# Kernel optimization log

Measured on AMD Instinct MI355X. Metric: run time of the kernel, lower is better.

Reference implementation:

```python
import jax, jax.numpy as jnp
import numpy as np

N_NODES = 100000
N_EDGES = 1600000
D_IN = 128
D_HID = 64


def setup_inputs() -> dict:
    key = jax.random.key(0)
    k1, k2, k3, k4 = jax.random.split(key, 4)
    x = jax.random.normal(k1, (N_NODES, D_IN), dtype=jnp.float32)
    edge_index = jax.random.randint(k2, (2, N_EDGES), 0, N_NODES, dtype=jnp.int64)
    W1 = jax.random.normal(k3, (D_IN, D_HID), dtype=jnp.float32) / np.sqrt(D_IN)
    b1 = jnp.zeros((D_HID,), dtype=jnp.float32)
    W2 = jax.random.normal(k4, (D_HID, 1), dtype=jnp.float32) / np.sqrt(D_HID)
    b2 = jnp.zeros((1,), dtype=jnp.float32)
    return {"x": x, "edge_index": edge_index, "W1": W1, "b1": b1, "W2": W2, "b2": b2}


def _gcn_layer(x, W, b, src, dst, norm, n):
    # PyG GCNConv: linear transform, then normalized scatter-add aggregation, then bias
    h = x @ W                                   # [N, d_out]
    msg = h[src] * norm[:, None]                # gather + edge-weight   [E', d_out]
    out = jax.ops.segment_sum(msg, dst, num_segments=n)  # scatter-add
    return out + b


def reference(x, edge_index, W1, b1, W2, b2):
    n = x.shape[0]
    loops = jnp.arange(n, dtype=edge_index.dtype)
    src = jnp.concatenate([edge_index[0], loops])  # self-loops added (GCN default)
    dst = jnp.concatenate([edge_index[1], loops])
    # symmetric normalization: deg^{-1/2}[src] * deg^{-1/2}[dst]
    deg = jax.ops.segment_sum(jnp.ones(dst.shape, x.dtype), dst, num_segments=n)
    dis = jnp.where(deg > 0, jax.lax.rsqrt(jnp.maximum(deg, 1e-12)), 0.0)
    norm = dis[src] * dis[dst]
    h = jax.nn.relu(_gcn_layer(x, W1, b1, src, dst, norm, n))
    y = _gcn_layer(h, W2, b2, src, dst, norm, n)   # [N, 1]
    # ConstantPad1d((0, num_node_features-1), 0) -> [N, D_IN]
    return jnp.pad(y, ((0, 0), (0, x.shape[1] - 1)))
```

## Files before the change

### kernel.cpp

```cpp
#include <hip/hip_runtime.h>

#define N_NODES 100000
#define N_EDGES 1600000
#define D_IN 128
#define D_HID 64

#define BKT_SHIFT 8
#define BKT_NODES 256
#define NB 391
#define NBLK 392
#define SLOT 32
#define SEG4 (SLOT / 4)
#define REG4 (NBLK * SEG4)
#define BKT_CAP 5120
#define OVF_CAP 8192

#define EST 512
#define BST 1024

typedef __attribute__((ext_vector_type(8))) short bf16x8;
typedef __attribute__((ext_vector_type(4))) float f32x4;

__device__ __forceinline__ unsigned short f2b(float f) {
    union { float f; unsigned u; } c; c.f = f;
    unsigned r = (c.u + 0x7FFFu + ((c.u >> 16) & 1u)) >> 16;
    return (unsigned short)r;
}
__device__ __forceinline__ float blo(unsigned u) { return __uint_as_float(u << 16); }
__device__ __forceinline__ float bhi(unsigned u) { return __uint_as_float(u & 0xffff0000u); }

__global__ __launch_bounds__(256) void k_prep(const float* __restrict__ W1,
                                              unsigned short* __restrict__ w1t,
                                              int* __restrict__ ovf_cnt) {
    int t = blockIdx.x * 256 + threadIdx.x;
    if (t == 0) ovf_cnt[0] = 0;
    int k = t >> 6, f = t & 63;
    w1t[f * D_IN + k] = f2b(W1[t]);
}

__global__ __launch_bounds__(EST) void k_escatter(const int* __restrict__ src,
                                                  const int* __restrict__ dst,
                                                  int* __restrict__ pairs,
                                                  int* __restrict__ cnt_blk,
                                                  int* __restrict__ ovf_cnt,
                                                  int2* __restrict__ ovf, int E) {
    __shared__ int lcur[NB];
    __shared__ int lp[NB * SLOT];
    int tid = threadIdx.x;
    for (int t = tid; t < NB; t += EST) lcur[t] = 0;
    __syncthreads();
    int chunk = (E + NBLK - 1) / NBLK;
    int beg = blockIdx.x * chunk;
    int end = min(beg + chunk, E);
    for (int e = beg + tid; e < end; e += EST) {
        int d = dst[e], s = src[e];
        int bk = d >> BKT_SHIFT;
        int slot = atomicAdd(&lcur[bk], 1);
        if (slot < SLOT)
            lp[(bk << 5) + slot] = (s << BKT_SHIFT) | (d & (BKT_NODES - 1));
        else {
            int o = atomicAdd(ovf_cnt, 1);
            if (o < OVF_CAP) ovf[o] = make_int2(s, d);
        }
    }
    __syncthreads();
    uint4* p4 = (uint4*)pairs;
    const uint4* lp4 = (const uint4*)lp;
    for (int i4 = tid; i4 < NB * SEG4; i4 += EST) {
        int bk = i4 >> 3;
        int c = min(lcur[bk], SLOT);
        if (((i4 & 7) << 2) < c)
            p4[((size_t)bk * NBLK + blockIdx.x) * SEG4 + (i4 & 7)] = lp4[i4];
    }
    for (int t = tid; t < NB; t += EST)
        cnt_blk[t * NBLK + blockIdx.x] = min(lcur[t], SLOT);
}

__global__ __launch_bounds__(BST) void k_bsort(const uint4* __restrict__ pairs4,
                                               const int* __restrict__ cnt_blk,
                                               const int* __restrict__ ovf_cnt,
                                               const int2* __restrict__ ovf,
                                               int* __restrict__ srcs_sorted,
                                               int* __restrict__ row_start,
                                               int* __restrict__ row_end,
                                               float* __restrict__ dis, int n) {
    __shared__ uint4 reg4[REG4];
    __shared__ int segc[NBLK];
    __shared__ int cnt[BKT_NODES];
    __shared__ int exc[BKT_NODES];
    __shared__ int sorted[BKT_CAP];
    __shared__ int nE_sh;
    int b = blockIdx.x;
    int tid = threadIdx.x;
    int node0 = b << BKT_SHIFT;
    int ocnt = min(ovf_cnt[0], OVF_CAP);
    const uint4* region = pairs4 + (size_t)b * REG4;

    for (int i = tid; i < NBLK; i += BST) segc[i] = cnt_blk[b * NBLK + i];
    if (tid < BKT_NODES) cnt[tid] = 0;
    __syncthreads();

    for (int i4 = tid; i4 < REG4; i4 += BST) {
        int c = segc[i4 >> 3];
        int k = (i4 & 7) * 4;
        if (k < c) {
            uint4 v = region[i4];
            reg4[i4] = v;
            atomicAdd(&cnt[v.x & (BKT_NODES - 1)], 1);
            if (k + 1 < c) atomicAdd(&cnt[v.y & (BKT_NODES - 1)], 1);
            if (k + 2 < c) atomicAdd(&cnt[v.z & (BKT_NODES - 1)], 1);
            if (k + 3 < c) atomicAdd(&cnt[v.w & (BKT_NODES - 1)], 1);
        }
    }
    for (int k = tid; k < ocnt; k += BST) {
        int2 e = ovf[k];
        if ((e.y >> BKT_SHIFT) == b) atomicAdd(&cnt[e.y & (BKT_NODES - 1)], 1);
    }
    __syncthreads();

    if (tid < 64) {
        int run = 0;
        for (int c = 0; c < BKT_NODES; c += 64) {
            int v = cnt[c + tid];
            int inc = v;
            for (int off = 1; off < 64; off <<= 1) {
                int t2 = __shfl_up(inc, off);
                if (tid >= off) inc += t2;
            }
            exc[c + tid] = run + inc - v;
            run += __shfl(inc, 63);
        }
        if (tid == 63) nE_sh = run;
    }
    __syncthreads();

    if (tid < BKT_NODES) {
        int node = node0 + tid;
        if (node < n) {
            int rs = b * BKT_CAP + exc[tid];
            row_start[node] = rs;
            row_end[node] = rs + cnt[tid];
            dis[node] = rsqrtf((float)cnt[tid] + 1.0f);
        }
    }
    int nE = nE_sh;
    __syncthreads();
    if (tid < BKT_NODES) cnt[tid] = exc[tid];
    __syncthreads();

    for (int i4 = tid; i4 < REG4; i4 += BST) {
        int c = segc[i4 >> 3];
        int k = (i4 & 7) * 4;
        if (k < c) {
            uint4 v = reg4[i4];
            { int p = atomicAdd(&cnt[v.x & (BKT_NODES - 1)], 1); sorted[p] = (int)(v.x >> 8); }
            if (k + 1 < c) { int p = atomicAdd(&cnt[v.y & (BKT_NODES - 1)], 1); sorted[p] = (int)(v.y >> 8); }
            if (k + 2 < c) { int p = atomicAdd(&cnt[v.z & (BKT_NODES - 1)], 1); sorted[p] = (int)(v.z >> 8); }
            if (k + 3 < c) { int p = atomicAdd(&cnt[v.w & (BKT_NODES - 1)], 1); sorted[p] = (int)(v.w >> 8); }
        }
    }
    for (int k = tid; k < ocnt; k += BST) {
        int2 e = ovf[k];
        if ((e.y >> BKT_SHIFT) == b) {
            int p = atomicAdd(&cnt[e.y & (BKT_NODES - 1)], 1);
            sorted[p] = e.x;
        }
    }
    __syncthreads();

    int gbase = b * BKT_CAP;
    for (int k = tid; k < nE; k += BST)
        srcs_sorted[gbase + k] = sorted[k];
}

#define LS 136
__global__ __launch_bounds__(256) void k_gemm1(const float* __restrict__ x,
                                               const uint4* __restrict__ w1t4,
                                               const float* __restrict__ dis,
                                               unsigned short* __restrict__ h1s, int n) {
    __shared__ unsigned short xs[64 * LS];
    __shared__ unsigned short ws[64 * LS];
    int tid = threadIdx.x;
    int node0 = blockIdx.x * 64;

#pragma unroll
    for (int it = 0; it < 4; ++it) {
        int e = tid + it * 256;
        int f = e >> 4, c = e & 15;
        *(uint4*)&ws[f * LS + c * 8] = w1t4[e];
    }
#pragma unroll
    for (int it = 0; it < 8; ++it) {
        int e4 = tid + it * 256;
        int node = e4 >> 5;
        int k = (e4 & 31) * 4;
        float4 v = make_float4(0.f, 0.f, 0.f, 0.f);
        if (node0 + node < n)
            v = ((const float4*)x)[((size_t)(node0 + node) * D_IN + k) >> 2];
        uint2 u;
        u.x = (unsigned)f2b(v.x) | ((unsigned)f2b(v.y) << 16);
        u.y = (unsigned)f2b(v.z) | ((unsigned)f2b(v.w) << 16);
        *(uint2*)&xs[node * LS + k] = u;
    }
    __syncthreads();

    int wv = tid >> 6;
    int lane = tid & 63;
    int m16 = lane & 15;
    int q = lane >> 4;

    bf16x8 afrag[4];
#pragma unroll
    for (int ks = 0; ks < 4; ++ks)
        afrag[ks] = *(const bf16x8*)&xs[(wv * 16 + m16) * LS + ks * 32 + q * 8];

    f32x4 acc[4];
#pragma unroll
    for (int ft = 0; ft < 4; ++ft) acc[ft] = (f32x4){0.f, 0.f, 0.f, 0.f};

#pragma unroll
    for (int ft = 0; ft < 4; ++ft)
#pragma unroll
        for (int ks = 0; ks < 4; ++ks) {
            bf16x8 bfrag = *(const bf16x8*)&ws[(ft * 16 + m16) * LS + ks * 32 + q * 8];
            acc[ft] = __builtin_amdgcn_mfma_f32_16x16x32_bf16(afrag[ks], bfrag, acc[ft], 0, 0, 0);
        }

#pragma unroll
    for (int r = 0; r < 4; ++r) {
        int node = node0 + wv * 16 + q * 4 + r;
        if (node < n) {
            float d = dis[node];
#pragma unroll
            for (int ft = 0; ft < 4; ++ft)
                h1s[(size_t)node * D_HID + ft * 16 + m16] = f2b(acc[ft][r] * d);
        }
    }
}

__global__ __launch_bounds__(256) void k_gather1(const int* __restrict__ srcs,
                                                 const int* __restrict__ row_start,
                                                 const int* __restrict__ row_end,
                                                 const float* __restrict__ dis,
                                                 const uint4* __restrict__ h4,
                                                 const float* __restrict__ b1,
                                                 const float* __restrict__ W2,
                                                 float* __restrict__ zd, int n) {
    int i = blockIdx.x * 8 + (threadIdx.x >> 5);
    int lane = threadIdx.x & 63;
    int g = (lane >> 3) & 3;
    int m8 = lane & 7;
    float dd = dis[i];

    float a0, a1, a2, a3, a4, a5, a6, a7;
    {
        uint4 u = h4[(unsigned)i * 8u + m8];
        float w = (g == 0) ? 1.f : 0.f;
        a0 = w * blo(u.x); a1 = w * bhi(u.x);
        a2 = w * blo(u.y); a3 = w * bhi(u.y);
        a4 = w * blo(u.z); a5 = w * bhi(u.z);
        a6 = w * blo(u.w); a7 = w * bhi(u.w);
    }

#define ACC(u) { a0 += blo(u.x); a1 += bhi(u.x); a2 += blo(u.y); a3 += bhi(u.y); \
                 a4 += blo(u.z); a5 += bhi(u.z); a6 += blo(u.w); a7 += bhi(u.w); }
    int end = row_end[i];
    int j = row_start[i] + g;
    for (; j + 12 < end; j += 16) {
        int s0 = srcs[j];
        int s1 = srcs[j + 4];
        int s2 = srcs[j + 8];
        int s3 = srcs[j + 12];
        uint4 u0 = h4[(unsigned)s0 * 8u + m8];
        uint4 u1 = h4[(unsigned)s1 * 8u + m8];
        uint4 u2 = h4[(unsigned)s2 * 8u + m8];
        uint4 u3 = h4[(unsigned)s3 * 8u + m8];
        ACC(u0); ACC(u1); ACC(u2); ACC(u3);
    }
    for (; j + 4 < end; j += 8) {
        int s0 = srcs[j];
        int s1 = srcs[j + 4];
        uint4 u0 = h4[(unsigned)s0 * 8u + m8];
        uint4 u1 = h4[(unsigned)s1 * 8u + m8];
        ACC(u0); ACC(u1);
    }
    if (j < end) {
        int s0 = srcs[j];
        uint4 u0 = h4[(unsigned)s0 * 8u + m8];
        ACC(u0);
    }
#undef ACC

#pragma unroll
    for (int off = 8; off < 32; off <<= 1) {
        a0 += __shfl_xor(a0, off); a1 += __shfl_xor(a1, off);
        a2 += __shfl_xor(a2, off); a3 += __shfl_xor(a3, off);
        a4 += __shfl_xor(a4, off); a5 += __shfl_xor(a5, off);
        a6 += __shfl_xor(a6, off); a7 += __shfl_xor(a7, off);
    }
    float4 ba = ((const float4*)b1)[m8 * 2];
    float4 bb = ((const float4*)b1)[m8 * 2 + 1];
    float4 wa = ((const float4*)W2)[m8 * 2];
    float4 wb = ((const float4*)W2)[m8 * 2 + 1];
    float v = fmaxf(fmaf(dd, a0, ba.x), 0.f) * wa.x + fmaxf(fmaf(dd, a1, ba.y), 0.f) * wa.y
            + fmaxf(fmaf(dd, a2, ba.z), 0.f) * wa.z + fmaxf(fmaf(dd, a3, ba.w), 0.f) * wa.w
            + fmaxf(fmaf(dd, a4, bb.x), 0.f) * wb.x + fmaxf(fmaf(dd, a5, bb.y), 0.f) * wb.y
            + fmaxf(fmaf(dd, a6, bb.z), 0.f) * wb.z + fmaxf(fmaf(dd, a7, bb.w), 0.f) * wb.w;
#pragma unroll
    for (int off = 1; off < 8; off <<= 1) v += __shfl_xor(v, off);
    if ((lane & 31) == 0) zd[i] = v * dd;
}

__global__ __launch_bounds__(256) void k_gather2(const int* __restrict__ srcs,
                                                 const int* __restrict__ row_start,
                                                 const int* __restrict__ row_end,
                                                 const float* __restrict__ dis,
                                                 const float* __restrict__ zd,
                                                 const float* __restrict__ b2,
                                                 float* __restrict__ out, int n) {
    int i = blockIdx.x * 8 + (threadIdx.x >> 5);
    int l = threadIdx.x & 31;
    float acc = 0.f;
    int beg = row_start[i], end = row_end[i];
    for (int j = beg + l; j < end; j += 32)
        acc += zd[srcs[j]];
#pragma unroll
    for (int off = 1; off < 32; off <<= 1) acc += __shfl_xor(acc, off);
    float y = (acc + zd[i]) * dis[i] + b2[0];
    float4 v = make_float4(0.f, 0.f, 0.f, 0.f);
    if (l == 0) v.x = y;
    ((float4*)out)[(size_t)i * 32 + l] = v;
}

extern "C" void kernel_launch(void* const* d_in, const int* in_sizes, int n_in,
                              void* d_out, int out_size, void* d_ws, size_t ws_size,
                              hipStream_t stream) {
    const float* x  = (const float*)d_in[0];
    const int*   ei = (const int*)d_in[1];
    const float* W1 = (const float*)d_in[2];
    const float* b1 = (const float*)d_in[3];
    const float* W2 = (const float*)d_in[4];
    const float* b2 = (const float*)d_in[5];
    float* out = (float*)d_out;

    const int n = N_NODES;
    const int E = N_EDGES;
    const int* src = ei;
    const int* dst = ei + E;

    int* pairs       = (int*)d_ws;
    int* cnt_blk     = pairs + (size_t)NB * NBLK * SLOT;
    int* srcs_sorted = cnt_blk + (size_t)NB * NBLK;
    int* row_start   = srcs_sorted + (size_t)NB * BKT_CAP;
    int* row_end     = row_start + n;
    int* ovf_cnt     = row_end + n;
    int2* ovf        = (int2*)(ovf_cnt + 4);
    float* dis       = (float*)(ovf + OVF_CAP);
    unsigned short* h1s = (unsigned short*)(dis + n);
    unsigned short* w1t = h1s + (size_t)n * D_HID;
    float* zd        = (float*)(w1t + D_IN * D_HID);

    k_prep<<<32, 256, 0, stream>>>(W1, w1t, ovf_cnt);
    k_escatter<<<NBLK, EST, 0, stream>>>(src, dst, pairs, cnt_blk, ovf_cnt, ovf, E);
    k_bsort<<<NB, BST, 0, stream>>>((const uint4*)pairs, cnt_blk, ovf_cnt, ovf,
                                    srcs_sorted, row_start, row_end, dis, n);

    k_gemm1<<<(n + 63) / 64, 256, 0, stream>>>(x, (const uint4*)w1t, dis, h1s, n);

    k_gather1<<<(n + 7) / 8, 256, 0, stream>>>(srcs_sorted, row_start, row_end, dis,
                                               (const uint4*)h1s, b1, W2, zd, n);
    k_gather2<<<(n + 7) / 8, 256, 0, stream>>>(srcs_sorted, row_start, row_end, dis,
                                               zd, b2, out, n);
}
```

Measured before the change: 195.3 us.

## Fuse edge scatter and GEMM into one launch, apply source norm in gather

The edge-bucketing scatter and the X·W1 bf16 MFMA GEMM now run as two block roles inside one kernel, so the GEMM no longer waits for the degree computation. To make that possible, the per-source dis scaling moves out of the GEMM epilogue and into gather1, which loads dis[src] per edge and uses FMA accumulation. The W1 transpose/convert prep kernel is folded into each GEMM block, and the overflow-counter reset becomes a memset. This removes two launches and overlaps independent work, at the cost of an extra scattered 4-byte load per edge in the gather and redundant W1 conversion in every GEMM block.

```diff
diff --git a/kernel.cpp b/kernel.cpp
--- a/kernel.cpp
+++ b/kernel.cpp
@@ -15,8 +15,9 @@
 #define BKT_CAP 5120
 #define OVF_CAP 8192
 
-#define EST 512
+#define FST 512
 #define BST 1024
+#define GEMM_NB 782
 
 typedef __attribute__((ext_vector_type(8))) short bf16x8;
 typedef __attribute__((ext_vector_type(4))) float f32x4;
@@ -29,51 +30,110 @@
 __device__ __forceinline__ float blo(unsigned u) { return __uint_as_float(u << 16); }
 __device__ __forceinline__ float bhi(unsigned u) { return __uint_as_float(u & 0xffff0000u); }
 
-__global__ __launch_bounds__(256) void k_prep(const float* __restrict__ W1,
-                                              unsigned short* __restrict__ w1t,
-                                              int* __restrict__ ovf_cnt) {
-    int t = blockIdx.x * 256 + threadIdx.x;
-    if (t == 0) ovf_cnt[0] = 0;
-    int k = t >> 6, f = t & 63;
-    w1t[f * D_IN + k] = f2b(W1[t]);
-}
-
-__global__ __launch_bounds__(EST) void k_escatter(const int* __restrict__ src,
-                                                  const int* __restrict__ dst,
-                                                  int* __restrict__ pairs,
-                                                  int* __restrict__ cnt_blk,
-                                                  int* __restrict__ ovf_cnt,
-                                                  int2* __restrict__ ovf, int E) {
-    __shared__ int lcur[NB];
-    __shared__ int lp[NB * SLOT];
+#define LS 136
+__global__ __launch_bounds__(FST) void k_fused(const int* __restrict__ src,
+                                               const int* __restrict__ dst,
+                                               int* __restrict__ pairs,
+                                               int* __restrict__ cnt_blk,
+                                               int* __restrict__ ovf_cnt,
+                                               int2* __restrict__ ovf, int E,
+                                               const float* __restrict__ x,
+                                               const float* __restrict__ W1,
+                                               unsigned short* __restrict__ h1s, int n) {
+    __shared__ __align__(16) unsigned char smem[52224];
     int tid = threadIdx.x;
-    for (int t = tid; t < NB; t += EST) lcur[t] = 0;
-    __syncthreads();
-    int chunk = (E + NBLK - 1) / NBLK;
-    int beg = blockIdx.x * chunk;
-    int end = min(beg + chunk, E);
-    for (int e = beg + tid; e < end; e += EST) {
-        int d = dst[e], s = src[e];
-        int bk = d >> BKT_SHIFT;
-        int slot = atomicAdd(&lcur[bk], 1);
-        if (slot < SLOT)
-            lp[(bk << 5) + slot] = (s << BKT_SHIFT) | (d & (BKT_NODES - 1));
-        else {
-            int o = atomicAdd(ovf_cnt, 1);
-            if (o < OVF_CAP) ovf[o] = make_int2(s, d);
-        }
-    }
-    __syncthreads();
-    uint4* p4 = (uint4*)pairs;
-    const uint4* lp4 = (const uint4*)lp;
-    for (int i4 = tid; i4 < NB * SEG4; i4 += EST) {
-        int bk = i4 >> 3;
-        int c = min(lcur[bk], SLOT);
-        if (((i4 & 7) << 2) < c)
-            p4[((size_t)bk * NBLK + blockIdx.x) * SEG4 + (i4 & 7)] = lp4[i4];
-    }
-    for (int t = tid; t < NB; t += EST)
-        cnt_blk[t * NBLK + blockIdx.x] = min(lcur[t], SLOT);
+
+    if (blockIdx.x < NBLK) {
+        int* lp   = (int*)smem;
+        int* lcur = lp + NB * SLOT;
+        for (int t = tid; t < NB; t += FST) lcur[t] = 0;
+        __syncthreads();
+        int chunk = (E + NBLK - 1) / NBLK;
+        int beg = blockIdx.x * chunk;
+        int end = min(beg + chunk, E);
+        for (int e = beg + tid; e < end; e += FST) {
+            int d = dst[e], s = src[e];
+            int bk = d >> BKT_SHIFT;
+            int slot = atomicAdd(&lcur[bk], 1);
+            if (slot < SLOT)
+                lp[(bk << 5) + slot] = (s << BKT_SHIFT) | (d & (BKT_NODES - 1));
+            else {
+                int o = atomicAdd(ovf_cnt, 1);
+                if (o < OVF_CAP) ovf[o] = make_int2(s, d);
+            }
+        }
+        __syncthreads();
+        uint4* p4 = (uint4*)pairs;
+        const uint4* lp4 = (const uint4*)lp;
+        for (int i4 = tid; i4 < NB * SEG4; i4 += FST) {
+            int bk = i4 >> 3;
+            int c = min(lcur[bk], SLOT);
+            if (((i4 & 7) << 2) < c)
+                p4[((size_t)bk * NBLK + blockIdx.x) * SEG4 + (i4 & 7)] = lp4[i4];
+        }
+        for (int t = tid; t < NB; t += FST)
+            cnt_blk[t * NBLK + blockIdx.x] = min(lcur[t], SLOT);
+    } else {
+        unsigned short* ws = (unsigned short*)smem;
+        unsigned short* xs = ws + 64 * LS;
+        int half = tid >> 8;
+        int t2 = tid & 255;
+        int node0 = (blockIdx.x - NBLK) * 128 + half * 64;
+        unsigned short* xsh = xs + half * 64 * LS;
+
+#pragma unroll
+        for (int it = 0; it < 16; ++it) {
+            int e = tid + it * 512;
+            int k = e >> 6, f = e & 63;
+            ws[f * LS + k] = f2b(W1[e]);
+        }
+#pragma unroll
+        for (int it = 0; it < 8; ++it) {
+            int e4 = t2 + it * 256;
+            int node = e4 >> 5;
+            int k = (e4 & 31) * 4;
+            float4 v = make_float4(0.f, 0.f, 0.f, 0.f);
+            if (node0 + node < n)
+                v = ((const float4*)x)[((size_t)(node0 + node) * D_IN + k) >> 2];
+            uint2 u;
+            u.x = (unsigned)f2b(v.x) | ((unsigned)f2b(v.y) << 16);
+            u.y = (unsigned)f2b(v.z) | ((unsigned)f2b(v.w) << 16);
+            *(uint2*)&xsh[node * LS + k] = u;
+        }
+        __syncthreads();
+
+        int wv = t2 >> 6;
+        int lane = t2 & 63;
+        int m16 = lane & 15;
+        int q = lane >> 4;
+
+        bf16x8 afrag[4];
+#pragma unroll
+        for (int ks = 0; ks < 4; ++ks)
+            afrag[ks] = *(const bf16x8*)&xsh[(wv * 16 + m16) * LS + ks * 32 + q * 8];
+
+        f32x4 acc[4];
+#pragma unroll
+        for (int ft = 0; ft < 4; ++ft) acc[ft] = (f32x4){0.f, 0.f, 0.f, 0.f};
+
+#pragma unroll
+        for (int ft = 0; ft < 4; ++ft)
+#pragma unroll
+            for (int ks = 0; ks < 4; ++ks) {
+                bf16x8 bfrag = *(const bf16x8*)&ws[(ft * 16 + m16) * LS + ks * 32 + q * 8];
+                acc[ft] = __builtin_amdgcn_mfma_f32_16x16x32_bf16(afrag[ks], bfrag, acc[ft], 0, 0, 0);
+            }
+
+#pragma unroll
+        for (int r = 0; r < 4; ++r) {
+            int node = node0 + wv * 16 + q * 4 + r;
+            if (node < n) {
+#pragma unroll
+                for (int ft = 0; ft < 4; ++ft)
+                    h1s[(size_t)node * D_HID + ft * 16 + m16] = f2b(acc[ft][r]);
+            }
+        }
+    }
 }
 
 __global__ __launch_bounds__(BST) void k_bsort(const uint4* __restrict__ pairs4,
@@ -173,71 +233,6 @@
         srcs_sorted[gbase + k] = sorted[k];
 }
 
-#define LS 136
-__global__ __launch_bounds__(256) void k_gemm1(const float* __restrict__ x,
-                                               const uint4* __restrict__ w1t4,
-                                               const float* __restrict__ dis,
-                                               unsigned short* __restrict__ h1s, int n) {
-    __shared__ unsigned short xs[64 * LS];
-    __shared__ unsigned short ws[64 * LS];
-    int tid = threadIdx.x;
-    int node0 = blockIdx.x * 64;
-
-#pragma unroll
-    for (int it = 0; it < 4; ++it) {
-        int e = tid + it * 256;
-        int f = e >> 4, c = e & 15;
-        *(uint4*)&ws[f * LS + c * 8] = w1t4[e];
-    }
-#pragma unroll
-    for (int it = 0; it < 8; ++it) {
-        int e4 = tid + it * 256;
-        int node = e4 >> 5;
-        int k = (e4 & 31) * 4;
-        float4 v = make_float4(0.f, 0.f, 0.f, 0.f);
-        if (node0 + node < n)
-            v = ((const float4*)x)[((size_t)(node0 + node) * D_IN + k) >> 2];
-        uint2 u;
-        u.x = (unsigned)f2b(v.x) | ((unsigned)f2b(v.y) << 16);
-        u.y = (unsigned)f2b(v.z) | ((unsigned)f2b(v.w) << 16);
-        *(uint2*)&xs[node * LS + k] = u;
-    }
-    __syncthreads();
-
-    int wv = tid >> 6;
-    int lane = tid & 63;
-    int m16 = lane & 15;
-    int q = lane >> 4;
-
-    bf16x8 afrag[4];
-#pragma unroll
-    for (int ks = 0; ks < 4; ++ks)
-        afrag[ks] = *(const bf16x8*)&xs[(wv * 16 + m16) * LS + ks * 32 + q * 8];
-
-    f32x4 acc[4];
-#pragma unroll
-    for (int ft = 0; ft < 4; ++ft) acc[ft] = (f32x4){0.f, 0.f, 0.f, 0.f};
-
-#pragma unroll
-    for (int ft = 0; ft < 4; ++ft)
-#pragma unroll
-        for (int ks = 0; ks < 4; ++ks) {
-            bf16x8 bfrag = *(const bf16x8*)&ws[(ft * 16 + m16) * LS + ks * 32 + q * 8];
-            acc[ft] = __builtin_amdgcn_mfma_f32_16x16x32_bf16(afrag[ks], bfrag, acc[ft], 0, 0, 0);
-        }
-
-#pragma unroll
-    for (int r = 0; r < 4; ++r) {
-        int node = node0 + wv * 16 + q * 4 + r;
-        if (node < n) {
-            float d = dis[node];
-#pragma unroll
-            for (int ft = 0; ft < 4; ++ft)
-                h1s[(size_t)node * D_HID + ft * 16 + m16] = f2b(acc[ft][r] * d);
-        }
-    }
-}
-
 __global__ __launch_bounds__(256) void k_gather1(const int* __restrict__ srcs,
                                                  const int* __restrict__ row_start,
                                                  const int* __restrict__ row_end,
@@ -255,15 +250,17 @@
     float a0, a1, a2, a3, a4, a5, a6, a7;
     {
         uint4 u = h4[(unsigned)i * 8u + m8];
-        float w = (g == 0) ? 1.f : 0.f;
+        float w = (g == 0) ? dd : 0.f;
         a0 = w * blo(u.x); a1 = w * bhi(u.x);
         a2 = w * blo(u.y); a3 = w * bhi(u.y);
         a4 = w * blo(u.z); a5 = w * bhi(u.z);
         a6 = w * blo(u.w); a7 = w * bhi(u.w);
     }
 
-#define ACC(u) { a0 += blo(u.x); a1 += bhi(u.x); a2 += blo(u.y); a3 += bhi(u.y); \
-                 a4 += blo(u.z); a5 += bhi(u.z); a6 += blo(u.w); a7 += bhi(u.w); }
+#define ACC(u, ds) { a0 = fmaf(ds, blo(u.x), a0); a1 = fmaf(ds, bhi(u.x), a1); \
+                     a2 = fmaf(ds, blo(u.y), a2); a3 = fmaf(ds, bhi(u.y), a3); \
+                     a4 = fmaf(ds, blo(u.z), a4); a5 = fmaf(ds, bhi(u.z), a5); \
+                     a6 = fmaf(ds, blo(u.w), a6); a7 = fmaf(ds, bhi(u.w), a7); }
     int end = row_end[i];
     int j = row_start[i] + g;
     for (; j + 12 < end; j += 16) {
@@ -271,23 +268,26 @@
         int s1 = srcs[j + 4];
         int s2 = srcs[j + 8];
         int s3 = srcs[j + 12];
+        float d0 = dis[s0], d1 = dis[s1], d2 = dis[s2], d3 = dis[s3];
         uint4 u0 = h4[(unsigned)s0 * 8u + m8];
         uint4 u1 = h4[(unsigned)s1 * 8u + m8];
         uint4 u2 = h4[(unsigned)s2 * 8u + m8];
         uint4 u3 = h4[(unsigned)s3 * 8u + m8];
-        ACC(u0); ACC(u1); ACC(u2); ACC(u3);
+        ACC(u0, d0); ACC(u1, d1); ACC(u2, d2); ACC(u3, d3);
     }
     for (; j + 4 < end; j += 8) {
         int s0 = srcs[j];
         int s1 = srcs[j + 4];
+        float d0 = dis[s0], d1 = dis[s1];
         uint4 u0 = h4[(unsigned)s0 * 8u + m8];
         uint4 u1 = h4[(unsigned)s1 * 8u + m8];
-        ACC(u0); ACC(u1);
+        ACC(u0, d0); ACC(u1, d1);
     }
     if (j < end) {
         int s0 = srcs[j];
+        float d0 = dis[s0];
         uint4 u0 = h4[(unsigned)s0 * 8u + m8];
-        ACC(u0);
+        ACC(u0, d0);
     }
 #undef ACC
 
@@ -357,16 +357,13 @@
     int2* ovf        = (int2*)(ovf_cnt + 4);
     float* dis       = (float*)(ovf + OVF_CAP);
     unsigned short* h1s = (unsigned short*)(dis + n);
-    unsigned short* w1t = h1s + (size_t)n * D_HID;
-    float* zd        = (float*)(w1t + D_IN * D_HID);
-
-    k_prep<<<32, 256, 0, stream>>>(W1, w1t, ovf_cnt);
-    k_escatter<<<NBLK, EST, 0, stream>>>(src, dst, pairs, cnt_blk, ovf_cnt, ovf, E);
+    float* zd        = (float*)(h1s + (size_t)n * D_HID);
+
+    hipMemsetAsync(ovf_cnt, 0, sizeof(int), stream);
+    k_fused<<<NBLK + GEMM_NB, FST, 0, stream>>>(src, dst, pairs, cnt_blk, ovf_cnt,
+                                                ovf, E, x, W1, h1s, n);
     k_bsort<<<NB, BST, 0, stream>>>((const uint4*)pairs, cnt_blk, ovf_cnt, ovf,
                                     srcs_sorted, row_start, row_end, dis, n);
-
-    k_gemm1<<<(n + 63) / 64, 256, 0, stream>>>(x, (const uint4*)w1t, dis, h1s, n);
-
     k_gather1<<<(n + 7) / 8, 256, 0, stream>>>(srcs_sorted, row_start, row_end, dis,
                                                (const uint4*)h1s, b1, W2, zd, n);
     k_gather2<<<(n + 7) / 8, 256, 0, stream>>>(srcs_sorted, row_start, row_end, dis,
```

New measurement: 194.0 us. No clear change (-0.7%).
